# Optimization experiments

Measured on AMD Instinct MI355X. Metric: run time of the kernel, lower is better.

Reference implementation:

```python
import jax, jax.numpy as jnp
import numpy as np

N = 100000
DIM = 128
M = 1600000
E = 200000
HOP = 2


def setup_inputs() -> dict:
    key = jax.random.key(0)
    k1, k2, k3, k4 = jax.random.split(key, 4)
    edge = jax.random.randint(k1, (2, E), 0, N, dtype=jnp.int64)
    adj_row = jax.random.randint(k2, (M,), 0, N, dtype=jnp.int64)
    adj_col = jax.random.randint(k3, (M,), 0, N, dtype=jnp.int64)
    # degree consistent with adjacency rows (clamped to >=1 to avoid 1/0)
    deg = jax.ops.segment_sum(jnp.ones((M,), jnp.float32), adj_row, num_segments=N)
    deg = jnp.maximum(deg, 1.0).reshape(N, 1)
    # 'gaussian' signature sampling: row-L2-normalized standard normal vectors
    g = jax.random.normal(k4, (N, DIM), dtype=jnp.float32)
    x_sig = g / jnp.linalg.norm(g, axis=1, keepdims=True)
    return {"edge": edge, "adj_row": adj_row, "adj_col": adj_col, "deg": deg, "x_sig": x_sig}


def reference(edge, adj_row, adj_col, deg, x_sig):
    n = deg.shape[0]
    D = x_sig.shape[1]
    degrev = 1.0 / deg  # [N,1]
    # x: [N, 3*D] -- raw / rsqrt(deg)-scaled / rsqrt(1+log(deg))-scaled signatures
    x = jnp.concatenate(
        [x_sig, x_sig * jax.lax.rsqrt(deg), x_sig * jax.lax.rsqrt(1.0 + jnp.log(deg))],
        axis=1,
    )

    def spmm(v):  # adj_t @ v via gather + segment-sum over nnz
        return jax.ops.segment_sum(v[adj_col], adj_row, num_segments=n)

    xs = [x, degrev * spmm(x)]
    for _ in range(2, HOP + 1):
        xs.append(degrev * spmm(xs[-1]) - xs[-2])
    # [N, K, D] with K = 3*(hop+1)
    X = jnp.concatenate(xs, axis=1).reshape(n, -1, D)
    a = X[edge[0]]  # [E, K, D]
    b = X[edge[1]]  # [E, K, D]
    ret = jnp.einsum("ekd,eld->ekl", a, b)  # [E, K, K]
    ret = ret + jnp.swapaxes(ret, 1, 2)
    return ret.reshape(ret.shape[0], -1)  # [E, K*K]
```

## Files before the change

### kernel.cpp

```cpp
#include <hip/hip_runtime.h>
#include <hip/hip_fp16.h>

#define D128 128
#define X19_STRIDE 768

typedef __attribute__((ext_vector_type(8))) _Float16 f16x8;
typedef __attribute__((ext_vector_type(4))) float    f32x4;

__global__ void k_scales(const float* __restrict__ deg, float* __restrict__ scales, int N) {
  int n = blockIdx.x * blockDim.x + threadIdx.x;
  if (n >= N) return;
  float dg = deg[n];
  scales[2 * n]     = rsqrtf(dg);
  scales[2 * n + 1] = rsqrtf(1.0f + logf(dg));
}

__global__ void k_hist(const int* __restrict__ row, int* __restrict__ cnt, int M) {
  int i = blockIdx.x * blockDim.x + threadIdx.x;
  if (i < M) atomicAdd(&cnt[row[i]], 1);
}

__global__ void __launch_bounds__(256)
k_blocksum(const int* __restrict__ cnt, int* __restrict__ bsum, int n) {
  __shared__ int ws[4];
  int base = blockIdx.x * 1024;
  int t = threadIdx.x;
  int s = 0;
  for (int j = t; j < 1024; j += 256) {
    int i = base + j;
    if (i < n) s += cnt[i];
  }
  #pragma unroll
  for (int d = 32; d >= 1; d >>= 1) s += __shfl_down(s, d);
  if ((t & 63) == 0) ws[t >> 6] = s;
  __syncthreads();
  if (t == 0) bsum[blockIdx.x] = ws[0] + ws[1] + ws[2] + ws[3];
}

__global__ void k_scan_bsums(const int* __restrict__ bsum, int* __restrict__ bpre,
                             int* __restrict__ off, int nb, int n) {
  if (threadIdx.x == 0 && blockIdx.x == 0) {
    int run = 0;
    for (int b = 0; b < nb; ++b) { bpre[b] = run; run += bsum[b]; }
    off[n] = run;
  }
}

__global__ void __launch_bounds__(1024)
k_scan_apply(const int* __restrict__ cnt, const int* __restrict__ bpre,
             int* __restrict__ off, int* __restrict__ cursor, int n) {
  __shared__ int warp_sums[16];
  int i = blockIdx.x * 1024 + threadIdx.x;
  int lane = threadIdx.x & 63;
  int wid  = threadIdx.x >> 6;
  int v = (i < n) ? cnt[i] : 0;
  int s = v;
  #pragma unroll
  for (int d = 1; d < 64; d <<= 1) {
    int t = __shfl_up(s, d);
    if (lane >= d) s += t;
  }
  if (lane == 63) warp_sums[wid] = s;
  __syncthreads();
  if (threadIdx.x < 16) {
    int ws = warp_sums[threadIdx.x];
    #pragma unroll
    for (int d = 1; d < 16; d <<= 1) {
      int t = __shfl_up(ws, d);
      if ((int)threadIdx.x >= d) ws += t;
    }
    warp_sums[threadIdx.x] = ws;
  }
  __syncthreads();
  int excl = (s - v) + (wid > 0 ? warp_sums[wid - 1] : 0) + bpre[blockIdx.x];
  if (i < n) { off[i] = excl; cursor[i] = excl; }
}

__global__ void k_scatter(const int* __restrict__ row, const int* __restrict__ col,
                          int* __restrict__ cursor, int* __restrict__ csr_col, int M) {
  int i = blockIdx.x * blockDim.x + threadIdx.x;
  if (i < M) {
    int r = row[i];
    int pos = atomicAdd(&cursor[r], 1);
    csr_col[pos] = col[i];
  }
}

__global__ void __launch_bounds__(D128)
k_spmm1(const float* __restrict__ x_sig, const float* __restrict__ scales,
        __half* __restrict__ X19,
        const int* __restrict__ off, const int* __restrict__ csr_col,
        const float* __restrict__ deg) {
  int r = blockIdx.x;
  int d = threadIdx.x;
  __shared__ int scol[D128];
  int start = off[r], end = off[r + 1];
  float a0 = 0.f, a1 = 0.f, a2 = 0.f;
  for (int b = start; b < end; b += D128) {
    int len = min(end - b, D128);
    if (d < len) scol[d] = csr_col[b + d];
    __syncthreads();
    for (int j = 0; j < len; ++j) {
      int c = scol[j];
      float v  = x_sig[(size_t)c * D128 + d];
      float s1 = scales[2 * c];
      float s2 = scales[2 * c + 1];
      a0 += v;
      a1 += v * s1;
      a2 += v * s2;
    }
    __syncthreads();
  }
  float dr = 1.0f / deg[r];
  size_t o = (size_t)r * X19_STRIDE;
  X19[o + d]       = __float2half(a0 * dr);
  X19[o + 128 + d] = __float2half(a1 * dr);
  X19[o + 256 + d] = __float2half(a2 * dr);
}

__global__ void __launch_bounds__(192)
k_spmm2(const float* __restrict__ x_sig, const float* __restrict__ scales,
        __half* __restrict__ X19,
        const int* __restrict__ off, const int* __restrict__ csr_col,
        const float* __restrict__ deg) {
  int r = blockIdx.x;
  int t = threadIdx.x;
  __shared__ int scol[192];
  int start = off[r], end = off[r + 1];
  float acc0 = 0.f, acc1 = 0.f;
  for (int b = start; b < end; b += 192) {
    int len = min(end - b, 192);
    if (t < len) scol[t] = csr_col[b + t];
    __syncthreads();
    for (int j = 0; j < len; ++j) {
      __half2 h = *reinterpret_cast<const __half2*>(
          X19 + (size_t)scol[j] * X19_STRIDE + 2 * t);
      float2 f = __half22float2(h);
      acc0 += f.x; acc1 += f.y;
    }
    __syncthreads();
  }
  float dr = 1.0f / deg[r];
  int e0 = 2 * t;
  int k = e0 >> 7, dd = e0 & 127;
  float2 xv = *reinterpret_cast<const float2*>(x_sig + (size_t)r * D128 + dd);
  float sk = (k == 0) ? 1.0f : ((k == 1) ? scales[2 * r] : scales[2 * r + 1]);
  __half2 o;
  o.x = __float2half(acc0 * dr - xv.x * sk);
  o.y = __float2half(acc1 * dr - xv.y * sk);
  *reinterpret_cast<__half2*>(X19 + (size_t)r * X19_STRIDE + 384 + e0) = o;
}

__global__ void __launch_bounds__(256)
k_edge(const float* __restrict__ x_sig, const float* __restrict__ scales,
       const __half* __restrict__ X19, const int* __restrict__ edge,
       float* __restrict__ out, int E) {
  __shared__ float Gs[4][81];
  int w    = threadIdx.x >> 6;
  int lane = threadIdx.x & 63;
  int e = blockIdx.x * 4 + w;
  int row = lane & 15;
  int kg  = lane >> 4;

  f32x4 acc = {0.f, 0.f, 0.f, 0.f};
  if (e < E) {
    int u = edge[e];
    int v = edge[E + e];
    float su = (row == 1) ? scales[2 * u] : ((row == 2) ? scales[2 * u + 1] : 1.0f);
    float sv = (row == 1) ? scales[2 * v] : ((row == 2) ? scales[2 * v + 1] : 1.0f);
    const float*  xu = x_sig + (size_t)u * D128;
    const float*  xv = x_sig + (size_t)v * D128;
    const __half* Xu = X19 + (size_t)u * X19_STRIDE;
    const __half* Xv = X19 + (size_t)v * X19_STRIDE;

    f16x8 a[4], b[4];
    if (row >= 9) {
      #pragma unroll
      for (int c = 0; c < 4; ++c)
        #pragma unroll
        for (int j = 0; j < 8; ++j) { a[c][j] = (_Float16)0.0f; b[c][j] = (_Float16)0.0f; }
    } else if (row < 3) {
      #pragma unroll
      for (int c = 0; c < 4; ++c) {
        int koff = c * 32 + kg * 8;
        float4 u0 = *reinterpret_cast<const float4*>(xu + koff);
        float4 u1 = *reinterpret_cast<const float4*>(xu + koff + 4);
        float4 v0 = *reinterpret_cast<const float4*>(xv + koff);
        float4 v1 = *reinterpret_cast<const float4*>(xv + koff + 4);
        a[c][0] = (_Float16)(u0.x * su); a[c][1] = (_Float16)(u0.y * su);
        a[c][2] = (_Float16)(u0.z * su); a[c][3] = (_Float16)(u0.w * su);
        a[c][4] = (_Float16)(u1.x * su); a[c][5] = (_Float16)(u1.y * su);
        a[c][6] = (_Float16)(u1.z * su); a[c][7] = (_Float16)(u1.w * su);
        b[c][0] = (_Float16)(v0.x * sv); b[c][1] = (_Float16)(v0.y * sv);
        b[c][2] = (_Float16)(v0.z * sv); b[c][3] = (_Float16)(v0.w * sv);
        b[c][4] = (_Float16)(v1.x * sv); b[c][5] = (_Float16)(v1.y * sv);
        b[c][6] = (_Float16)(v1.z * sv); b[c][7] = (_Float16)(v1.w * sv);
      }
    } else {
      const __half* pu = Xu + (row - 3) * D128;
      const __half* pv = Xv + (row - 3) * D128;
      #pragma unroll
      for (int c = 0; c < 4; ++c) {
        int koff = c * 32 + kg * 8;
        a[c] = *reinterpret_cast<const f16x8*>(pu + koff);
        b[c] = *reinterpret_cast<const f16x8*>(pv + koff);
      }
    }
    #pragma unroll
    for (int c = 0; c < 4; ++c)
      acc = __builtin_amdgcn_mfma_f32_16x16x32_f16(a[c], b[c], acc, 0, 0, 0);

    #pragma unroll
    for (int j = 0; j < 4; ++j) {
      int r = kg * 4 + j;
      if (r < 9 && row < 9) Gs[w][r * 9 + row] = acc[j];
    }
  }
  __syncthreads();
  if (e < E) {
    for (int t = lane; t < 81; t += 64) {
      int k = t / 9, l = t % 9;
      out[(size_t)e * 81 + t] = Gs[w][t] + Gs[w][l * 9 + k];
    }
  }
}

extern "C" void kernel_launch(void* const* d_in, const int* in_sizes, int n_in,
                              void* d_out, int out_size, void* d_ws, size_t ws_size,
                              hipStream_t stream) {
  const int*   edge    = (const int*)d_in[0];
  const int*   adj_row = (const int*)d_in[1];
  const int*   adj_col = (const int*)d_in[2];
  const float* deg     = (const float*)d_in[3];
  const float* x_sig   = (const float*)d_in[4];
  float* out = (float*)d_out;

  const int E = in_sizes[0] / 2;
  const int M = in_sizes[1];
  const int N = in_sizes[3];
  const int NCHUNK = (N + 1023) / 1024;

  size_t x19_elems = (size_t)N * X19_STRIDE;
  size_t need = x19_elems * 2
              + (2 * (size_t)N) * 4
              + ((size_t)(N + 1) + (size_t)N + (size_t)M) * 4
              + 2 * (size_t)NCHUNK * 4;
  if (ws_size < need) return;

  __half* X19   = (__half*)d_ws;
  float* scales = (float*)(X19 + x19_elems);
  int* off      = (int*)(scales + 2 * (size_t)N);
  int* cursor   = off + (N + 1);
  int* csr_col  = cursor + N;
  int* bsum     = csr_col + M;
  int* bpre     = bsum + NCHUNK;

  hipMemsetAsync(cursor, 0, (size_t)N * sizeof(int), stream);

  k_scales<<<(N + 255) / 256, 256, 0, stream>>>(deg, scales, N);
  k_hist<<<(M + 255) / 256, 256, 0, stream>>>(adj_row, cursor, M);
  k_blocksum<<<NCHUNK, 256, 0, stream>>>(cursor, bsum, N);
  k_scan_bsums<<<1, 64, 0, stream>>>(bsum, bpre, off, NCHUNK, N);
  k_scan_apply<<<NCHUNK, 1024, 0, stream>>>(cursor, bpre, off, cursor, N);
  k_scatter<<<(M + 255) / 256, 256, 0, stream>>>(adj_row, adj_col, cursor, csr_col, M);

  k_spmm1<<<N, D128, 0, stream>>>(x_sig, scales, X19, off, csr_col, deg);
  k_spmm2<<<N, 192, 0, stream>>>(x_sig, scales, X19, off, csr_col, deg);

  k_edge<<<(E + 3) / 4, 256, 0, stream>>>(x_sig, scales, X19, edge, out, E);
}
```

Measured before the change: 807.3 us.

## Use wave-per-row SpMM with shuffled indices and pack two edges per MFMA

Both SpMM kernels now assign one 64-lane wavefront per row, four rows per block. Column indices are broadcast with shuffles instead of shared memory plus block barriers, and each lane accumulates two features across all three channels. The edge kernel packs two edges into one 16x16 MFMA using a reduced 7x7 Gram matrix, since the three scaled copies of x_sig are linearly dependent. The per-node rsqrt scales are applied afterwards in the output epilogue. This halves the MFMA count and the redundant x_sig loads, but adds more complex indexing and per-element scaling in the output loop.

```diff
diff --git a/kernel.cpp b/kernel.cpp
--- a/kernel.cpp
+++ b/kernel.cpp
@@ -86,141 +86,136 @@
   }
 }
 
-__global__ void __launch_bounds__(D128)
+__global__ void __launch_bounds__(256)
 k_spmm1(const float* __restrict__ x_sig, const float* __restrict__ scales,
         __half* __restrict__ X19,
         const int* __restrict__ off, const int* __restrict__ csr_col,
-        const float* __restrict__ deg) {
-  int r = blockIdx.x;
-  int d = threadIdx.x;
-  __shared__ int scol[D128];
+        const float* __restrict__ deg, int N) {
+  int r = blockIdx.x * 4 + (threadIdx.x >> 6);
+  if (r >= N) return;
+  int lane = threadIdx.x & 63;
+  int d0 = lane * 2;
   int start = off[r], end = off[r + 1];
-  float a0 = 0.f, a1 = 0.f, a2 = 0.f;
-  for (int b = start; b < end; b += D128) {
-    int len = min(end - b, D128);
-    if (d < len) scol[d] = csr_col[b + d];
-    __syncthreads();
+  float a0x = 0.f, a0y = 0.f, a1x = 0.f, a1y = 0.f, a2x = 0.f, a2y = 0.f;
+  for (int b = start; b < end; b += 64) {
+    int len = min(end - b, 64);
+    int ci = (lane < len) ? csr_col[b + lane] : 0;
     for (int j = 0; j < len; ++j) {
-      int c = scol[j];
-      float v  = x_sig[(size_t)c * D128 + d];
-      float s1 = scales[2 * c];
-      float s2 = scales[2 * c + 1];
-      a0 += v;
-      a1 += v * s1;
-      a2 += v * s2;
-    }
-    __syncthreads();
+      int c = __shfl(ci, j);
+      float2 v = *reinterpret_cast<const float2*>(x_sig + (size_t)c * D128 + d0);
+      float2 s = *reinterpret_cast<const float2*>(scales + 2 * c);
+      a0x += v.x;        a0y += v.y;
+      a1x += v.x * s.x;  a1y += v.y * s.x;
+      a2x += v.x * s.y;  a2y += v.y * s.y;
+    }
   }
   float dr = 1.0f / deg[r];
-  size_t o = (size_t)r * X19_STRIDE;
-  X19[o + d]       = __float2half(a0 * dr);
-  X19[o + 128 + d] = __float2half(a1 * dr);
-  X19[o + 256 + d] = __float2half(a2 * dr);
-}
-
-__global__ void __launch_bounds__(192)
+  __half* o = X19 + (size_t)r * X19_STRIDE + d0;
+  *reinterpret_cast<__half2*>(o)       = __floats2half2_rn(a0x * dr, a0y * dr);
+  *reinterpret_cast<__half2*>(o + 128) = __floats2half2_rn(a1x * dr, a1y * dr);
+  *reinterpret_cast<__half2*>(o + 256) = __floats2half2_rn(a2x * dr, a2y * dr);
+}
+
+__global__ void __launch_bounds__(256)
 k_spmm2(const float* __restrict__ x_sig, const float* __restrict__ scales,
         __half* __restrict__ X19,
         const int* __restrict__ off, const int* __restrict__ csr_col,
-        const float* __restrict__ deg) {
-  int r = blockIdx.x;
-  int t = threadIdx.x;
-  __shared__ int scol[192];
+        const float* __restrict__ deg, int N) {
+  int r = blockIdx.x * 4 + (threadIdx.x >> 6);
+  if (r >= N) return;
+  int lane = threadIdx.x & 63;
+  int d0 = lane * 2;
   int start = off[r], end = off[r + 1];
-  float acc0 = 0.f, acc1 = 0.f;
-  for (int b = start; b < end; b += 192) {
-    int len = min(end - b, 192);
-    if (t < len) scol[t] = csr_col[b + t];
-    __syncthreads();
+  float s0x = 0.f, s0y = 0.f, s1x = 0.f, s1y = 0.f, s2x = 0.f, s2y = 0.f;
+  for (int b = start; b < end; b += 64) {
+    int len = min(end - b, 64);
+    int ci = (lane < len) ? csr_col[b + lane] : 0;
     for (int j = 0; j < len; ++j) {
-      __half2 h = *reinterpret_cast<const __half2*>(
-          X19 + (size_t)scol[j] * X19_STRIDE + 2 * t);
-      float2 f = __half22float2(h);
-      acc0 += f.x; acc1 += f.y;
-    }
-    __syncthreads();
+      int c = __shfl(ci, j);
+      const __half* base = X19 + (size_t)c * X19_STRIDE + d0;
+      float2 v0 = __half22float2(*reinterpret_cast<const __half2*>(base));
+      float2 v1 = __half22float2(*reinterpret_cast<const __half2*>(base + 128));
+      float2 v2 = __half22float2(*reinterpret_cast<const __half2*>(base + 256));
+      s0x += v0.x; s0y += v0.y;
+      s1x += v1.x; s1y += v1.y;
+      s2x += v2.x; s2y += v2.y;
+    }
   }
   float dr = 1.0f / deg[r];
-  int e0 = 2 * t;
-  int k = e0 >> 7, dd = e0 & 127;
-  float2 xv = *reinterpret_cast<const float2*>(x_sig + (size_t)r * D128 + dd);
-  float sk = (k == 0) ? 1.0f : ((k == 1) ? scales[2 * r] : scales[2 * r + 1]);
-  __half2 o;
-  o.x = __float2half(acc0 * dr - xv.x * sk);
-  o.y = __float2half(acc1 * dr - xv.y * sk);
-  *reinterpret_cast<__half2*>(X19 + (size_t)r * X19_STRIDE + 384 + e0) = o;
+  float2 xv = *reinterpret_cast<const float2*>(x_sig + (size_t)r * D128 + d0);
+  float2 sc = *reinterpret_cast<const float2*>(scales + 2 * r);
+  __half* o = X19 + (size_t)r * X19_STRIDE + 384 + d0;
+  *reinterpret_cast<__half2*>(o)       = __floats2half2_rn(s0x * dr - xv.x,        s0y * dr - xv.y);
+  *reinterpret_cast<__half2*>(o + 128) = __floats2half2_rn(s1x * dr - xv.x * sc.x, s1y * dr - xv.y * sc.x);
+  *reinterpret_cast<__half2*>(o + 256) = __floats2half2_rn(s2x * dr - xv.x * sc.y, s2y * dr - xv.y * sc.y);
 }
 
 __global__ void __launch_bounds__(256)
 k_edge(const float* __restrict__ x_sig, const float* __restrict__ scales,
        const __half* __restrict__ X19, const int* __restrict__ edge,
        float* __restrict__ out, int E) {
-  __shared__ float Gs[4][81];
+  __shared__ float Gs[4][2][49];
   int w    = threadIdx.x >> 6;
   int lane = threadIdx.x & 63;
-  int e = blockIdx.x * 4 + w;
+  long e0 = ((long)blockIdx.x * 4 + w) * 2;
   int row = lane & 15;
   int kg  = lane >> 4;
+  int f   = min(row & 7, 6);
+  long ea = e0 + ((row >> 3) & 1);
+  bool va = ea < E;
+  int u = va ? edge[ea] : 0;
+  int v = va ? edge[E + ea] : 0;
+  const float*  xu = x_sig + (size_t)u * D128;
+  const float*  xv = x_sig + (size_t)v * D128;
+  const __half* Xu = X19 + (size_t)u * X19_STRIDE + (f - 1) * D128;
+  const __half* Xv = X19 + (size_t)v * X19_STRIDE + (f - 1) * D128;
 
   f32x4 acc = {0.f, 0.f, 0.f, 0.f};
-  if (e < E) {
-    int u = edge[e];
-    int v = edge[E + e];
-    float su = (row == 1) ? scales[2 * u] : ((row == 2) ? scales[2 * u + 1] : 1.0f);
-    float sv = (row == 1) ? scales[2 * v] : ((row == 2) ? scales[2 * v + 1] : 1.0f);
-    const float*  xu = x_sig + (size_t)u * D128;
-    const float*  xv = x_sig + (size_t)v * D128;
-    const __half* Xu = X19 + (size_t)u * X19_STRIDE;
-    const __half* Xv = X19 + (size_t)v * X19_STRIDE;
-
-    f16x8 a[4], b[4];
-    if (row >= 9) {
-      #pragma unroll
-      for (int c = 0; c < 4; ++c)
-        #pragma unroll
-        for (int j = 0; j < 8; ++j) { a[c][j] = (_Float16)0.0f; b[c][j] = (_Float16)0.0f; }
-    } else if (row < 3) {
-      #pragma unroll
-      for (int c = 0; c < 4; ++c) {
-        int koff = c * 32 + kg * 8;
-        float4 u0 = *reinterpret_cast<const float4*>(xu + koff);
-        float4 u1 = *reinterpret_cast<const float4*>(xu + koff + 4);
-        float4 v0 = *reinterpret_cast<const float4*>(xv + koff);
-        float4 v1 = *reinterpret_cast<const float4*>(xv + koff + 4);
-        a[c][0] = (_Float16)(u0.x * su); a[c][1] = (_Float16)(u0.y * su);
-        a[c][2] = (_Float16)(u0.z * su); a[c][3] = (_Float16)(u0.w * su);
-        a[c][4] = (_Float16)(u1.x * su); a[c][5] = (_Float16)(u1.y * su);
-        a[c][6] = (_Float16)(u1.z * su); a[c][7] = (_Float16)(u1.w * su);
-        b[c][0] = (_Float16)(v0.x * sv); b[c][1] = (_Float16)(v0.y * sv);
-        b[c][2] = (_Float16)(v0.z * sv); b[c][3] = (_Float16)(v0.w * sv);
-        b[c][4] = (_Float16)(v1.x * sv); b[c][5] = (_Float16)(v1.y * sv);
-        b[c][6] = (_Float16)(v1.z * sv); b[c][7] = (_Float16)(v1.w * sv);
-      }
+  #pragma unroll
+  for (int c = 0; c < 4; ++c) {
+    int koff = c * 32 + kg * 8;
+    f16x8 a, b;
+    if (f == 0) {
+      float4 u0 = *reinterpret_cast<const float4*>(xu + koff);
+      float4 u1 = *reinterpret_cast<const float4*>(xu + koff + 4);
+      float4 v0 = *reinterpret_cast<const float4*>(xv + koff);
+      float4 v1 = *reinterpret_cast<const float4*>(xv + koff + 4);
+      a[0] = (_Float16)u0.x; a[1] = (_Float16)u0.y; a[2] = (_Float16)u0.z; a[3] = (_Float16)u0.w;
+      a[4] = (_Float16)u1.x; a[5] = (_Float16)u1.y; a[6] = (_Float16)u1.z; a[7] = (_Float16)u1.w;
+      b[0] = (_Float16)v0.x; b[1] = (_Float16)v0.y; b[2] = (_Float16)v0.z; b[3] = (_Float16)v0.w;
+      b[4] = (_Float16)v1.x; b[5] = (_Float16)v1.y; b[6] = (_Float16)v1.z; b[7] = (_Float16)v1.w;
     } else {
-      const __half* pu = Xu + (row - 3) * D128;
-      const __half* pv = Xv + (row - 3) * D128;
-      #pragma unroll
-      for (int c = 0; c < 4; ++c) {
-        int koff = c * 32 + kg * 8;
-        a[c] = *reinterpret_cast<const f16x8*>(pu + koff);
-        b[c] = *reinterpret_cast<const f16x8*>(pv + koff);
-      }
-    }
-    #pragma unroll
-    for (int c = 0; c < 4; ++c)
-      acc = __builtin_amdgcn_mfma_f32_16x16x32_f16(a[c], b[c], acc, 0, 0, 0);
-
-    #pragma unroll
-    for (int j = 0; j < 4; ++j) {
-      int r = kg * 4 + j;
-      if (r < 9 && row < 9) Gs[w][r * 9 + row] = acc[j];
-    }
-  }
-  __syncthreads();
-  if (e < E) {
+      a = *reinterpret_cast<const f16x8*>(Xu + koff);
+      b = *reinterpret_cast<const f16x8*>(Xv + koff);
+    }
+    acc = __builtin_amdgcn_mfma_f32_16x16x32_f16(a, b, acc, 0, 0, 0);
+  }
+  #pragma unroll
+  for (int j = 0; j < 4; ++j) {
+    int cr = kg * 4 + j;
+    int cc = row;
+    if (cr < 7 && cc < 7)                       Gs[w][0][cr * 7 + cc] = acc[j];
+    else if (cr >= 8 && cr < 15 && cc >= 8 && cc < 15)
+                                                Gs[w][1][(cr - 8) * 7 + (cc - 8)] = acc[j];
+  }
+  __syncthreads();
+  #pragma unroll
+  for (int ee = 0; ee < 2; ++ee) {
+    long e = e0 + ee;
+    if (e >= E) break;
+    int uu = edge[e], vv = edge[E + e];
+    float su1 = scales[2 * uu], su2 = scales[2 * uu + 1];
+    float sv1 = scales[2 * vv], sv2 = scales[2 * vv + 1];
+    const float* G = Gs[w][ee];
     for (int t = lane; t < 81; t += 64) {
       int k = t / 9, l = t % 9;
-      out[(size_t)e * 81 + t] = Gs[w][t] + Gs[w][l * 9 + k];
+      int kp = (k < 3) ? 0 : k - 2;
+      int lp = (l < 3) ? 0 : l - 2;
+      float ak = (k == 1) ? su1 : ((k == 2) ? su2 : 1.f);
+      float al = (l == 1) ? su1 : ((l == 2) ? su2 : 1.f);
+      float bk = (k == 1) ? sv1 : ((k == 2) ? sv2 : 1.f);
+      float bl = (l == 1) ? sv1 : ((l == 2) ? sv2 : 1.f);
+      out[(size_t)e * 81 + t] = ak * bl * G[kp * 7 + lp] + al * bk * G[lp * 7 + kp];
     }
   }
 }
@@ -264,8 +259,8 @@
   k_scan_apply<<<NCHUNK, 1024, 0, stream>>>(cursor, bpre, off, cursor, N);
   k_scatter<<<(M + 255) / 256, 256, 0, stream>>>(adj_row, adj_col, cursor, csr_col, M);
 
-  k_spmm1<<<N, D128, 0, stream>>>(x_sig, scales, X19, off, csr_col, deg);
-  k_spmm2<<<N, 192, 0, stream>>>(x_sig, scales, X19, off, csr_col, deg);
-
-  k_edge<<<(E + 3) / 4, 256, 0, stream>>>(x_sig, scales, X19, edge, out, E);
-}
+  k_spmm1<<<(N + 3) / 4, 256, 0, stream>>>(x_sig, scales, X19, off, csr_col, deg, N);
+  k_spmm2<<<(N + 3) / 4, 256, 0, stream>>>(x_sig, scales, X19, off, csr_col, deg, N);
+
+  k_edge<<<(E + 7) / 8, 256, 0, stream>>>(x_sig, scales, X19, edge, out, E);
+}
```

Result: faster. 759.2 us (-5.9%).
